# Kernel optimization log

Measured on AMD Instinct MI355X. Metric: run time of the kernel, lower is better.

Reference implementation:

```python
import jax, jax.numpy as jnp
import numpy as np
from jax import lax

K_SQ = 8  # scaling-and-squaring steps (GridExp default)


def lrelu(x):
    return jnp.where(x >= 0, x, 0.2 * x)


def conv(x, w, b, stride=1):
    y = lax.conv_general_dilated(x, w, (stride,) * 3, 'SAME',
                                 dimension_numbers=('NCDHW', 'OIDHW', 'NCDHW'))
    return y + b[None, :, None, None, None]


def convt(x, w, b):
    y = lax.conv_transpose(x, w, (2, 2, 2), 'SAME',
                           dimension_numbers=('NCDHW', 'OIDHW', 'NCDHW'))
    return y + b[None, :, None, None, None]


def identity_grid(shape):
    rng = [jnp.arange(s, dtype=jnp.float32) for s in shape]
    return jnp.stack(jnp.meshgrid(*rng, indexing='ij'), axis=-1)


def pull_one(img, grid, extrapolate):
    # img (C, X, Y, Z); grid (..., 3) in voxel coordinates; trilinear sampling
    X, Y, Z = img.shape[1:]
    g0f = jnp.floor(grid)
    w = grid - g0f
    g0 = g0f.astype(jnp.int32)
    flat = img.reshape(img.shape[0], -1)
    out = jnp.zeros(img.shape[:1] + grid.shape[:-1], img.dtype)
    for dx in (0, 1):
        for dy in (0, 1):
            for dz in (0, 1):
                ix = jnp.clip(g0[..., 0] + dx, 0, X - 1)
                iy = jnp.clip(g0[..., 1] + dy, 0, Y - 1)
                iz = jnp.clip(g0[..., 2] + dz, 0, Z - 1)
                idx = (ix * Y + iy) * Z + iz
                val = jnp.take(flat, idx.reshape(-1), axis=1).reshape(out.shape)
                wgt = ((w[..., 0] if dx else 1 - w[..., 0]) *
                       (w[..., 1] if dy else 1 - w[..., 1]) *
                       (w[..., 2] if dz else 1 - w[..., 2]))
                out = out + wgt[None] * val
    if not extrapolate:  # zero outside the field of view (GridPull extrapolate=False)
        inb = ((grid[..., 0] >= 0) & (grid[..., 0] <= X - 1) &
               (grid[..., 1] >= 0) & (grid[..., 1] <= Y - 1) &
               (grid[..., 2] >= 0) & (grid[..., 2] <= Z - 1))
        out = out * inb[None]
    return out


pull_batch = jax.vmap(pull_one, in_axes=(0, 0, None))


def resize_field(field, out_shape, value_scale):
    # field (B, X, Y, Z, D) channel-last; trilinear resize (align-centers), scale values
    in_shape = field.shape[1:-1]
    coords = identity_grid(out_shape)
    scale = jnp.array([(i - 1) / (o - 1) for i, o in zip(in_shape, out_shape)], jnp.float32)
    coords = coords * scale
    f = jnp.moveaxis(field, -1, 1)
    cb = jnp.broadcast_to(coords, (field.shape[0],) + coords.shape)
    out = pull_batch(f, cb, True)
    return jnp.moveaxis(out, 1, -1) * value_scale


def affine_basis_cso():
    # CSO in 3D: 3 translations + 3 rotations + 1 isotropic zoom -> 7 params
    B = np.zeros((7, 4, 4), np.float32)
    for i in range(3):
        B[i, i, 3] = 1.0
    for k, (i, j) in enumerate([(0, 1), (0, 2), (1, 2)]):
        B[3 + k, i, j] = 1.0
        B[3 + k, j, i] = -1.0
    for i in range(3):
        B[6, i, i] = 1.0
    return jnp.asarray(B)


def forward_core(source, target, cnn_w, cnn_b, enc_w, enc_b, up_w, up_b, dec_w, dec_b, fin_w, fin_b):
    x = jnp.concatenate([source, target], axis=1)  # (B, 2, X, Y, Z)
    # ---- affine head CNN: 4 strided convs + head conv + global reduction -> (B, 7)
    h = x
    for i in range(4):
        h = lrelu(conv(h, cnn_w[i], cnn_b[i], stride=2))
    h = conv(h, cnn_w[4], cnn_b[4])
    aff_prm = h.mean(axis=(2, 3, 4))
    # ---- UNet velocity head -> (B, X, Y, Z, 3)
    skips = [x]
    h = x
    for i in range(4):
        h = lrelu(conv(h, enc_w[i], enc_b[i], stride=2))
        skips.append(h)
    for i in range(4):
        h = lrelu(convt(h, up_w[i], up_b[i]))
        h = jnp.concatenate([h, skips[3 - i]], axis=1)
        h = lrelu(conv(h, dec_w[i], dec_b[i]))
    vel = jnp.moveaxis(conv(h, fin_w, fin_b), 1, -1)
    shape = vel.shape[1:-1]
    small = tuple(s // 2 for s in shape)
    # ---- exp(): downsample velocity (displacement: values scaled by 0.5)
    v_small = resize_field(vel, small, 0.5)
    idg = identity_grid(small)
    d = v_small / (2.0 ** K_SQ)
    for _ in range(K_SQ):  # scaling and squaring: d <- d + d o (id + d)
        d = d + jnp.moveaxis(pull_batch(jnp.moveaxis(d, -1, 1), idg[None] + d, True), 1, -1)
    grid = resize_field(idg[None] + d, shape, 2.0)  # grid: coords scaled by 2
    # ---- affine exponential, re-centered composition
    basis = affine_basis_cso()
    A = jax.vmap(lambda p: jax.scipy.linalg.expm(jnp.einsum('k,kij->ij', p, basis)))(aff_prm)
    shift = jnp.eye(4, dtype=jnp.float32).at[:3, 3].set(-jnp.asarray(shape, jnp.float32) / 2)
    A = jnp.linalg.solve(shift[None], A @ shift[None])  # inv(shift) @ A @ shift
    lin, off = A[:, :3, :3], A[:, :3, 3]
    grid = jnp.einsum('bij,bxyzj->bxyzi', lin, grid) + off[:, None, None, None, :]
    # ---- warp source
    deformed = pull_batch(source, grid, False)
    return deformed, vel, aff_prm


def setup_inputs() -> dict:
    key = jax.random.key(0)
    ks = iter(jax.random.split(key, 48))

    def p(shape):
        return jax.random.normal(next(ks), shape, jnp.float32) * 0.05

    d = {}
    d['source'] = jax.random.normal(next(ks), (1, 1, 96, 96, 96), jnp.float32)
    d['target'] = jax.random.normal(next(ks), (1, 1, 96, 96, 96), jnp.float32)
    for i, (o, c) in enumerate([(16, 2), (32, 16), (32, 32), (32, 32), (7, 32)]):
        d[f'cnn_w{i}'] = p((o, c, 3, 3, 3)); d[f'cnn_b{i}'] = p((o,))
    for i, (o, c) in enumerate([(16, 2), (32, 16), (32, 32), (32, 32)]):
        d[f'enc_w{i}'] = p((o, c, 3, 3, 3)); d[f'enc_b{i}'] = p((o,))
    for i, (o, c) in enumerate([(32, 32), (32, 32), (32, 32), (16, 32)]):
        d[f'up_w{i}'] = p((o, c, 3, 3, 3)); d[f'up_b{i}'] = p((o,))
    for i, (o, c) in enumerate([(32, 64), (32, 64), (32, 48), (16, 18)]):
        d[f'dec_w{i}'] = p((o, c, 3, 3, 3)); d[f'dec_b{i}'] = p((o,))
    d['fin_w'] = p((3, 16, 3, 3, 3)); d['fin_b'] = p((3,))
    return d


def reference(source, target,
              cnn_w0, cnn_b0, cnn_w1, cnn_b1, cnn_w2, cnn_b2, cnn_w3, cnn_b3, cnn_w4, cnn_b4,
              enc_w0, enc_b0, enc_w1, enc_b1, enc_w2, enc_b2, enc_w3, enc_b3,
              up_w0, up_b0, up_w1, up_b1, up_w2, up_b2, up_w3, up_b3,
              dec_w0, dec_b0, dec_w1, dec_b1, dec_w2, dec_b2, dec_w3, dec_b3,
              fin_w, fin_b):
    return forward_core(
        source, target,
        [cnn_w0, cnn_w1, cnn_w2, cnn_w3, cnn_w4], [cnn_b0, cnn_b1, cnn_b2, cnn_b3, cnn_b4],
        [enc_w0, enc_w1, enc_w2, enc_w3], [enc_b0, enc_b1, enc_b2, enc_b3],
        [up_w0, up_w1, up_w2, up_w3], [up_b0, up_b1, up_b2, up_b3],
        [dec_w0, dec_w1, dec_w2, dec_w3], [dec_b0, dec_b1, dec_b2, dec_b3],
        fin_w, fin_b)
```

## Files before the change

### kernel.cpp

```cpp
#include <hip/hip_runtime.h>

#define N96 884736
#define N48 110592
#define N24 13824
#define N12 1728
#define N6  216

typedef __attribute__((ext_vector_type(4))) short short4v;
typedef __attribute__((ext_vector_type(8))) short short8v;
typedef __attribute__((ext_vector_type(4))) float f32x4;

static __device__ __forceinline__ float lrelu_f(float x){ return x >= 0.f ? x : 0.2f*x; }
static __device__ __forceinline__ int clampi(int v,int lo,int hi){ return v<lo?lo:(v>hi?hi:v); }

static __device__ __forceinline__ short f2bf(float x){
    unsigned u = __builtin_bit_cast(unsigned, x);
    unsigned r = (u + 0x7FFFu + ((u >> 16) & 1u)) >> 16;
    return (short)r;
}

template<int OCPB, int S, bool RELU>
static __device__ __forceinline__ void conv_body(
    const float* __restrict__ in1, int C1,
    const float* __restrict__ in2, int C2,
    const float* __restrict__ w, const float* __restrict__ b,
    float* __restrict__ out, int ID, int OD,
    long out_cstride, int out_vmul, int t, int oc0)
{
    int i2 = t % OD; int r = t / OD; int i1 = r % OD; int i0 = r / OD;

    float acc[OCPB];
    #pragma unroll
    for (int j=0; j<OCPB; ++j) acc[j] = b[oc0+j];

    int zz[3], yy[3], xx[3]; bool zv[3], yv[3], xv[3];
    #pragma unroll
    for (int k=0; k<3; ++k){
        int a0 = (S==2) ? (2*i0+k) : (i0+k-1);
        int a1 = (S==2) ? (2*i1+k) : (i1+k-1);
        int a2 = (S==2) ? (2*i2+k) : (i2+k-1);
        zz[k]=a0; zv[k]=(a0>=0)&&(a0<ID);
        yy[k]=a1; yv[k]=(a1>=0)&&(a1<ID);
        xx[k]=a2; xv[k]=(a2>=0)&&(a2<ID);
    }
    const int C = C1 + C2;
    const int ID2 = ID*ID;
    const long ID3 = (long)ID2*ID;

    for (int s=0; s<2; ++s){
        const float* ip = s ? in2 : in1;
        int Cs  = s ? C2 : C1;
        int icb = s ? C1 : 0;
        if (Cs == 0) continue;
        for (int ic=0; ic<Cs; ++ic){
            const float* ipb = ip + (long)ic*ID3;
            float v[27];
            #pragma unroll
            for (int kd=0; kd<3; ++kd)
            #pragma unroll
            for (int kh=0; kh<3; ++kh)
            #pragma unroll
            for (int kw=0; kw<3; ++kw){
                bool ok = zv[kd] && yv[kh] && xv[kw];
                v[kd*9+kh*3+kw] = ok ? ipb[(long)zz[kd]*ID2 + yy[kh]*ID + xx[kw]] : 0.f;
            }
            const float* wbase = w + ((long)oc0*C + (icb+ic))*27;
            #pragma unroll
            for (int j=0; j<OCPB; ++j){
                const float* wo = wbase + (long)j*C*27;
                float sacc = 0.f;
                #pragma unroll
                for (int k=0; k<27; ++k) sacc += wo[k]*v[k];
                acc[j] += sacc;
            }
        }
    }
    #pragma unroll
    for (int j=0; j<OCPB; ++j){
        float o = RELU ? lrelu_f(acc[j]) : acc[j];
        out[(long)(oc0+j)*out_cstride + (long)t*out_vmul] = o;
    }
}

template<int OCPB, int S, bool RELU>
__global__ void conv3d_k(const float* __restrict__ in1, int C1,
                         const float* __restrict__ in2, int C2,
                         const float* __restrict__ w, const float* __restrict__ b,
                         float* __restrict__ out, int ID, int OD,
                         long out_cstride, int out_vmul)
{
    int nvox = OD*OD*OD;
    int t = blockIdx.x*blockDim.x + threadIdx.x;
    if (t >= nvox) return;
    conv_body<OCPB,S,RELU>(in1,C1,in2,C2,w,b,out,ID,OD,out_cstride,out_vmul,t,blockIdx.y*OCPB);
}

template<int OCPB, int S, bool RELU>
__global__ void conv3d_dual_k(const float* __restrict__ in1A, const float* __restrict__ in2A,
                              const float* __restrict__ in1B, const float* __restrict__ in2B,
                              int C1, int C2,
                              const float* __restrict__ wA, const float* __restrict__ bA,
                              const float* __restrict__ wB, const float* __restrict__ bB,
                              float* __restrict__ outA, float* __restrict__ outB,
                              int ID, int OD)
{
    int nvox = OD*OD*OD;
    int t = blockIdx.x*blockDim.x + threadIdx.x;
    if (t >= nvox) return;
    long nv = nvox;
    if (blockIdx.z == 0)
        conv_body<OCPB,S,RELU>(in1A,C1,in2A,C2,wA,bA,outA,ID,OD,nv,1,t,blockIdx.y*OCPB);
    else
        conv_body<OCPB,S,RELU>(in1B,C1,in2B,C2,wB,bB,outB,ID,OD,nv,1,t,blockIdx.y*OCPB);
}

__global__ void e0cl16_k(const float* __restrict__ e0, short* __restrict__ cl){
    int t = blockIdx.x*blockDim.x + threadIdx.x;
    if (t >= N48) return;
    short8v v0, v1;
    #pragma unroll
    for (int c=0;c<8;++c){ v0[c] = f2bf(e0[(long)c*N48 + t]); v1[c] = f2bf(e0[(long)(8+c)*N48 + t]); }
    *(short8v*)(cl + (long)t*16)     = v0;
    *(short8v*)(cl + (long)t*16 + 8) = v1;
}

__global__ __launch_bounds__(256, 2)
void conv_s2mfma_k(const short* __restrict__ cl,
                   const short* __restrict__ pack,
                   const float* __restrict__ b,
                   float* __restrict__ out)
{
    const short8v zero8 = {0,0,0,0,0,0,0,0};
    int lane = threadIdx.x & 63;
    int nb = gridDim.x;
    int bid = blockIdx.x;
    int sb = (bid & 7)*(nb >> 3) + (bid >> 3);
    int wid = sb*4 + (threadIdx.x >> 6);
    int ot = wid & 1;
    int s  = wid >> 1;
    int l15 = lane & 15, g = lane >> 4;
    int vL = s*16 + l15;
    int xL = vL % 24; int rL = vL/24; int yL = rL % 24; int zL = rL/24;
    const bool gok = (g < 2);

    float bias = b[ot*16 + l15];
    f32x4 acc = {bias,bias,bias,bias};

    #pragma unroll
    for (int kz=0; kz<3; ++kz){
        int iz = 2*zL + kz; bool okz = (iz < 48);
        int izc = okz ? iz : 0;
        #pragma unroll
        for (int ky=0; ky<3; ++ky){
            int iy = 2*yL + ky; bool oky = (iy < 48);
            int iyc = oky ? iy : 0;
            #pragma unroll
            for (int kx=0; kx<3; ++kx){
                int ix = 2*xL + kx; bool okx = (ix < 48);
                int ixc = okx ? ix : 0;
                bool ok = okz && oky && okx && gok;
                long base = (((long)izc*48 + iyc)*48 + ixc)*16 + (gok ? 8*g : 0);
                short8v a = *(const short8v*)(cl + base);
                if (!ok) a = zero8;
                int kidx = kz*9 + ky*3 + kx;
                short8v wfr = *(const short8v*)(pack + (((long)ot*27 + kidx)*64 + lane)*8);
                acc = __builtin_amdgcn_mfma_f32_16x16x32_bf16(a, wfr, acc, 0, 0, 0);
            }
        }
    }

    int oc = ot*16 + l15;
    #pragma unroll
    for (int reg=0; reg<4; ++reg){
        int m = 4*g + reg;
        out[(long)oc*N24 + s*16 + m] = lrelu_f(acc[reg]);
    }
}

__global__ void e3cl_k(const float* __restrict__ e3, short* __restrict__ cl){
    int t = blockIdx.x*blockDim.x + threadIdx.x;
    if (t >= N6) return;
    #pragma unroll
    for (int grp=0; grp<4; ++grp){
        short8v v;
        #pragma unroll
        for (int c=0;c<8;++c) v[c] = f2bf(e3[(long)(8*grp+c)*N6 + t]);
        *(short8v*)(cl + (long)t*32 + 8*grp) = v;
    }
}

__global__ void fill_e0_k(const float* __restrict__ e0, short* __restrict__ cl){
    int t = blockIdx.x*blockDim.x + threadIdx.x;
    if (t >= N48) return;
    short8v v0, v1;
    #pragma unroll
    for (int c=0;c<8;++c)  v0[c] = f2bf(e0[(long)c*N48 + t]);
    #pragma unroll
    for (int c=0;c<8;++c)  v1[c] = f2bf(e0[(long)(8+c)*N48 + t]);
    short8v z = {0,0,0,0,0,0,0,0};
    *(short8v*)(cl + (long)t*64 + 32) = v0;
    *(short8v*)(cl + (long)t*64 + 40) = v1;
    *(short8v*)(cl + (long)t*64 + 48) = z;
    *(short8v*)(cl + (long)t*64 + 56) = z;
}

template<int NV>
__global__ void fill_skip32_k(const float* __restrict__ e, short* __restrict__ cl){
    int t = blockIdx.x*blockDim.x + threadIdx.x;
    if (t >= NV) return;
    #pragma unroll
    for (int grp=0; grp<4; ++grp){
        short8v v;
        #pragma unroll
        for (int c=0;c<8;++c) v[c] = f2bf(e[(long)(8*grp+c)*NV + t]);
        *(short8v*)(cl + (long)t*64 + 32 + 8*grp) = v;
    }
}

static __device__ __forceinline__ void pack_std_d(const float* __restrict__ w, short* __restrict__ pack,
                                                  int t, int CREAL, int OCREAL){
    int kidx = t >> 6, lane = t & 63;
    int oc = lane & 15, g = lane >> 4;
    short8v f;
    #pragma unroll
    for (int j=0;j<8;++j){
        int ic = 8*g + j;
        float val = (oc < OCREAL && ic < CREAL) ? w[((long)oc*CREAL + ic)*27 + kidx] : 0.f;
        f[j] = f2bf(val);
    }
    *(short8v*)(pack + (long)t*8) = f;
}
static __device__ __forceinline__ void pack_2x2_d(const float* __restrict__ w, short* __restrict__ pack,
                                                  int t, int C){
    int lane = t & 63;
    int r = t >> 6;
    int kidx = r % 27;
    int kt = (r/27) & 1;
    int ot = r/54;
    int oc = ot*16 + (lane & 15), g = lane >> 4;
    short8v f;
    #pragma unroll
    for (int j=0;j<8;++j){
        int ic = kt*32 + 8*g + j;
        float val = (ic < C) ? w[((long)oc*C + ic)*27 + kidx] : 0.f;
        f[j] = f2bf(val);
    }
    *(short8v*)(pack + (long)t*8) = f;
}
static __device__ __forceinline__ void pack_up_d(const float* __restrict__ w, short* __restrict__ pack, int t){
    int lane = t & 63;
    int r = t >> 6;
    int kidx = r % 27;
    int ot = r/27;
    int oc = ot*16 + (lane & 15), g = lane >> 4;
    short8v f;
    #pragma unroll
    for (int j=0;j<8;++j){
        int ic = 8*g + j;
        f[j] = f2bf(w[((long)oc*32 + ic)*27 + kidx]);
    }
    *(short8v*)(pack + (long)t*8) = f;
}
static __device__ __forceinline__ void pack_s2_d(const float* __restrict__ w, short* __restrict__ pack, int t){
    int lane = t & 63;
    int r = t >> 6;
    int kidx = r % 27;
    int ot = r/27;
    int oc = ot*16 + (lane & 15), g = lane >> 4;
    short8v f;
    #pragma unroll
    for (int j=0;j<8;++j){
        int ic = 8*g + j;
        float val = (ic < 16) ? w[((long)oc*16 + ic)*27 + kidx] : 0.f;
        f[j] = f2bf(val);
    }
    *(short8v*)(pack + (long)t*8) = f;
}

__global__ void pack_all_k(const float* __restrict__ dw3, const float* __restrict__ fw,
                           const float* __restrict__ uw3,
                           const float* __restrict__ dw2, const float* __restrict__ dw1,
                           const float* __restrict__ dw0,
                           const float* __restrict__ uw2, const float* __restrict__ uw1,
                           const float* __restrict__ uw0,
                           const float* __restrict__ ew1,
                           short* __restrict__ PK3, short* __restrict__ PKF, short* __restrict__ PKU,
                           short* __restrict__ PK2, short* __restrict__ PK1, short* __restrict__ PK0,
                           short* __restrict__ PKU2, short* __restrict__ PKU1, short* __restrict__ PKU0,
                           short* __restrict__ PKE1)
{
    int t = blockIdx.x*blockDim.x + threadIdx.x;
    const int S1 = 27*64;
    const int S4 = 4*27*64;
    const int S2 = 2*27*64;
    if (t < S1){ pack_std_d(dw3, PK3, t, 18, 16); return; } t -= S1;
    if (t < S1){ pack_std_d(fw,  PKF, t, 16,  3); return; } t -= S1;
    if (t < S1){ pack_std_d(uw3, PKU, t, 32, 16); return; } t -= S1;
    if (t < S4){ pack_2x2_d(dw2, PK2, t, 48); return; } t -= S4;
    if (t < S4){ pack_2x2_d(dw1, PK1, t, 64); return; } t -= S4;
    if (t < S4){ pack_2x2_d(dw0, PK0, t, 64); return; } t -= S4;
    if (t < S2){ pack_up_d(uw2, PKU2, t); return; } t -= S2;
    if (t < S2){ pack_up_d(uw1, PKU1, t); return; } t -= S2;
    if (t < S2){ pack_up_d(uw0, PKU0, t); return; } t -= S2;
    if (t < S2){ pack_s2_d(ew1, PKE1, t); return; }
}

template<int CSTR, int OCREAL, bool RELU, int OMODE>
__global__ __launch_bounds__(256, 4)
void conv_mfma2_k(const short* __restrict__ cl,
                  const short* __restrict__ pack,
                  const float* __restrict__ b,
                  void* __restrict__ outp)
{
    const int D2 = 96*96;
    const short8v zero8 = {0,0,0,0,0,0,0,0};
    __shared__ short lwfr[27*64*8];
    for (int idx = threadIdx.x; idx < 27*64; idx += 256)
        *(short8v*)(lwfr + (long)idx*8) = *(const short8v*)(pack + (long)idx*8);
    __syncthreads();

    int lane = threadIdx.x & 63;
    int nb = gridDim.x;
    int bid = blockIdx.x;
    int sb = (bid & 7)*(nb >> 3) + (bid >> 3);
    int wid = sb*4 + (threadIdx.x >> 6);
    int l15 = lane & 15, g = lane >> 4;
    int xh = wid & 1;
    int rem = wid >> 1;
    int y = rem % 96;
    int z = (rem / 96)*2;
    int x0b = xh*48;
    const bool gok = (8*g < CSTR);
    const int go = gok ? 8*g : 0;

    float bias = (l15 < OCREAL) ? b[l15] : 0.f;
    f32x4 acc[2][3];
    #pragma unroll
    for (int o=0;o<2;++o)
    #pragma unroll
    for (int i=0;i<3;++i) acc[o][i] = (f32x4){bias,bias,bias,bias};

    #pragma unroll
    for (int dzr=-1; dzr<=2; ++dzr){
        int zz = z + dzr;
        bool okz = (zz>=0) && (zz<96);
        int zc = okz ? zz : z;
        #pragma unroll
        for (int dy=-1; dy<=1; ++dy){
            int yy = y+dy;
            bool okrow = okz && (yy>=0) && (yy<96);
            int yc = (yy>=0 && yy<96) ? yy : y;
            long rowb = (long)zc*D2 + (long)yc*96;
            #pragma unroll
            for (int dx=-1; dx<=1; ++dx){
                short8v a[3];
                #pragma unroll
                for (int i=0;i<3;++i){
                    int x = x0b + 16*i + l15 + dx;
                    bool okx = (x>=0) && (x<96);
                    int xc = okx ? x : (x0b + 16*i + l15);
                    a[i] = *(const short8v*)(cl + (rowb + xc)*CSTR + go);
                    bool oka = okrow && okx && gok;
                    if (!oka) a[i] = zero8;
                }
                if (dzr >= -1 && dzr <= 1){
                    int kidx = (dzr+1)*9 + (dy+1)*3 + (dx+1);
                    short8v wfr = *(const short8v*)(lwfr + ((long)kidx*64 + lane)*8);
                    #pragma unroll
                    for (int i=0;i<3;++i)
                        acc[0][i] = __builtin_amdgcn_mfma_f32_16x16x32_bf16(a[i], wfr, acc[0][i], 0, 0, 0);
                }
                if (dzr >= 0 && dzr <= 2){
                    int kidx = (dzr)*9 + (dy+1)*3 + (dx+1);
                    short8v wfr = *(const short8v*)(lwfr + ((long)kidx*64 + lane)*8);
                    #pragma unroll
                    for (int i=0;i<3;++i)
                        acc[1][i] = __builtin_amdgcn_mfma_f32_16x16x32_bf16(a[i], wfr, acc[1][i], 0, 0, 0);
                }
            }
        }
    }

    #pragma unroll
    for (int o=0;o<2;++o){
        long vrow = (long)(z+o)*D2 + (long)y*96 + x0b;
        if (OMODE == 0){
            short* op = (short*)outp;
            #pragma unroll
            for (int i=0;i<3;++i)
            #pragma unroll
            for (int reg=0; reg<4; ++reg){
                int mr = 4*g + reg;
                float v = RELU ? lrelu_f(acc[o][i][reg]) : acc[o][i][reg];
                op[(vrow + 16*i + mr)*16 + l15] = f2bf(v);
            }
        } else {
            float* op = (float*)outp;
            if (l15 < 3){
                #pragma unroll
                for (int i=0;i<3;++i)
                #pragma unroll
                for (int reg=0; reg<4; ++reg){
                    int mr = 4*g + reg;
                    op[(vrow + 16*i + mr)*3 + l15] = acc[o][i][reg];
                }
            }
        }
    }
}

__global__ __launch_bounds__(256, 2)
void conv_mfma48_k(const short* __restrict__ cl,
                   const short* __restrict__ pack,
                   const float* __restrict__ b,
                   short* __restrict__ out)
{
    const int D2 = 48*48;
    const short8v zero8 = {0,0,0,0,0,0,0,0};
    int lane = threadIdx.x & 63;
    int nb = gridDim.x;
    int bid = blockIdx.x;
    int sb = (bid & 7)*(nb >> 3) + (bid >> 3);
    int wid = sb*4 + (threadIdx.x >> 6);
    int l15 = lane & 15, g = lane >> 4;
    int y = wid % 48, z = wid / 48;

    float bias0 = b[l15];
    float bias1 = b[16 + l15];
    f32x4 acc[2][3];
    #pragma unroll
    for (int i=0;i<3;++i){ acc[0][i] = (f32x4){bias0,bias0,bias0,bias0};
                           acc[1][i] = (f32x4){bias1,bias1,bias1,bias1}; }

    #pragma unroll
    for (int dz=-1; dz<=1; ++dz){
        int zz = z+dz;
        bool okz = (zz>=0) && (zz<48);
        int zc = okz ? zz : z;
        #pragma unroll
        for (int dy=-1; dy<=1; ++dy){
            int yy = y+dy;
            bool okzy = okz && (yy>=0) && (yy<48);
            int yc = (yy>=0 && yy<48) ? yy : y;
            long rowb = (long)zc*D2 + (long)yc*48;
            #pragma unroll
            for (int dx=-1; dx<=1; ++dx){
                int kidx = (dz+1)*9 + (dy+1)*3 + (dx+1);
                #pragma unroll
                for (int kt=0; kt<2; ++kt){
                    short8v a[3];
                    #pragma unroll
                    for (int i=0;i<3;++i){
                        int x = 16*i + l15 + dx;
                        bool okx = (x>=0) && (x<48);
                        int xc = okx ? x : (16*i + l15);
                        a[i] = *(const short8v*)(cl + ((rowb + xc)*64 + kt*32 + 8*g));
                        if (!okx) a[i] = zero8;
                    }
                    #pragma unroll
                    for (int ot=0; ot<2; ++ot){
                        short8v wfr = *(const short8v*)(pack + (((long)(ot*2+kt)*27 + kidx)*64 + lane)*8);
                        if (!okzy) wfr = zero8;
                        #pragma unroll
                        for (int i=0;i<3;++i)
                            acc[ot][i] = __builtin_amdgcn_mfma_f32_16x16x32_bf16(a[i], wfr, acc[ot][i], 0, 0, 0);
                    }
                }
            }
        }
    }

    long vrow = (long)z*D2 + (long)y*48;
    #pragma unroll
    for (int ot=0; ot<2; ++ot)
    #pragma unroll
    for (int i=0;i<3;++i)
    #pragma unroll
    for (int reg=0; reg<4; ++reg){
        int mr = 4*g + reg;
        out[(vrow + 16*i + mr)*32 + ot*16 + l15] = f2bf(lrelu_f(acc[ot][i][reg]));
    }
}

template<int D>
__global__ __launch_bounds__(256, 2)
void conv_mfmaD_k(const short* __restrict__ cl,
                  const short* __restrict__ pack,
                  const float* __restrict__ b,
                  short* __restrict__ out)
{
    const short8v zero8 = {0,0,0,0,0,0,0,0};
    int lane = threadIdx.x & 63;
    int nb = gridDim.x;
    int bid = blockIdx.x;
    int sb = ((nb & 7) == 0) ? ((bid & 7)*(nb >> 3) + (bid >> 3)) : bid;
    int wid = sb*4 + (threadIdx.x >> 6);
    int ot = wid & 1;
    int s  = wid >> 1;
    int l15 = lane & 15, g = lane >> 4;
    int vL = s*16 + l15;
    int xL = vL % D; int rL = vL/D; int yL = rL % D; int zL = rL/D;

    float bias = b[ot*16 + l15];
    f32x4 acc = {bias,bias,bias,bias};

    #pragma unroll
    for (int dz=-1; dz<=1; ++dz){
        int iz = zL+dz; bool okz = (iz>=0)&&(iz<D); int izc = okz?iz:zL;
        #pragma unroll
        for (int dy=-1; dy<=1; ++dy){
            int iy = yL+dy; bool oky = (iy>=0)&&(iy<D); int iyc = oky?iy:yL;
            #pragma unroll
            for (int dx=-1; dx<=1; ++dx){
                int ix = xL+dx; bool okx = (ix>=0)&&(ix<D); int ixc = okx?ix:xL;
                bool ok = okz && oky && okx;
                long base = (((long)izc*D + iyc)*D + ixc)*64;
                int kidx = (dz+1)*9 + (dy+1)*3 + (dx+1);
                #pragma unroll
                for (int kt=0; kt<2; ++kt){
                    short8v wfr = *(const short8v*)(pack + (((long)(ot*2+kt)*27 + kidx)*64 + lane)*8);
                    short8v a = *(const short8v*)(cl + base + kt*32 + 8*g);
                    if (!ok) a = zero8;
                    acc = __builtin_amdgcn_mfma_f32_16x16x32_bf16(a, wfr, acc, 0, 0, 0);
                }
            }
        }
    }

    #pragma unroll
    for (int reg=0; reg<4; ++reg){
        int m = 4*g + reg;
        out[(long)(s*16 + m)*32 + ot*16 + l15] = f2bf(lrelu_f(acc[reg]));
    }
}

template<int IDI, int NST>
__global__ __launch_bounds__(256, 2)
void convt_mfmaup_k(const short* __restrict__ cl,
                    const short* __restrict__ pack,
                    const float* __restrict__ b,
                    short* __restrict__ o)
{
    const int D2i = IDI*IDI;
    const int OD = 2*IDI;
    const long D2o = (long)OD*OD;
    int lane = threadIdx.x & 63;
    int nb = gridDim.x;
    int bid = blockIdx.x;
    int sb = ((nb & 7) == 0) ? ((bid & 7)*(nb >> 3) + (bid >> 3)) : bid;
    int wid = sb*4 + (threadIdx.x >> 6);
    int px = wid & 1;
    int row = wid >> 1;
    int y = row % OD, z = row / OD;
    int l15 = lane & 15, g = lane >> 4;
    int pz = z & 1, py = y & 1, hz = z >> 1, hy = y >> 1;

    float bias0 = b[l15], bias1 = b[16 + l15];
    f32x4 acc[2][NST];
    #pragma unroll
    for (int i=0;i<NST;++i){ acc[0][i] = (f32x4){bias0,bias0,bias0,bias0};
                             acc[1][i] = (f32x4){bias1,bias1,bias1,bias1}; }

    int k0s[2], izs[2], nz=0;
    if (pz){ k0s[0]=1; izs[0]=hz; nz=1; }
    else { if (hz>=1){ k0s[nz]=0; izs[nz]=hz-1; ++nz; } k0s[nz]=2; izs[nz]=hz; ++nz; }
    int k1s[2], iys[2], ny=0;
    if (py){ k1s[0]=1; iys[0]=hy; ny=1; }
    else { if (hy>=1){ k1s[ny]=0; iys[ny]=hy-1; ++ny; } k1s[ny]=2; iys[ny]=hy; ++ny; }

    for (int a=0;a<nz;++a)
    for (int c=0;c<ny;++c){
        long rowb = (long)izs[a]*D2i + (long)iys[c]*IDI;
        int kbase = k0s[a]*9 + k1s[c]*3;
        int nqx = px?1:2;
        for (int qx=0; qx<nqx; ++qx){
            int k2 = px ? 1 : 2*qx;
            int xoff = px ? 0 : (qx-1);
            short8v av[NST];
            #pragma unroll
            for (int i=0;i<NST;++i){
                int ix = 16*i + l15 + xoff;
                av[i] = (short8v){0,0,0,0,0,0,0,0};
                if (ix >= 0 && ix < IDI) av[i] = *(const short8v*)(cl + ((rowb + ix)*32 + 8*g));
            }
            #pragma unroll
            for (int ot=0; ot<2; ++ot){
                short8v wfr = *(const short8v*)(pack + (((long)ot*27 + kbase + k2)*64 + lane)*8);
                #pragma unroll
                for (int i=0;i<NST;++i)
                    acc[ot][i] = __builtin_amdgcn_mfma_f32_16x16x32_bf16(av[i], wfr, acc[ot][i], 0, 0, 0);
            }
        }
    }

    #pragma unroll
    for (int ot=0; ot<2; ++ot)
    #pragma unroll
    for (int i=0;i<NST;++i)
    #pragma unroll
    for (int reg=0; reg<4; ++reg){
        int m = 16*i + 4*g + reg;
        if (m < IDI){
            long vox = (long)z*D2o + (long)y*OD + (2*m + px);
            o[vox*64 + ot*16 + l15] = f2bf(lrelu_f(acc[ot][i][reg]));
        }
    }
}

__global__ __launch_bounds__(256, 2)
void convt_mfma96_k(const short* __restrict__ cl,
                    const short* __restrict__ pack,
                    const float* __restrict__ b,
                    const float* __restrict__ src,
                    const float* __restrict__ tgt,
                    short* __restrict__ o)
{
    const int D2i = 48*48;
    const long D2o = 96*96;
    int lane = threadIdx.x & 63;
    int nb = gridDim.x;
    int bid = blockIdx.x;
    int sb = (bid & 7)*(nb >> 3) + (bid >> 3);
    int wid = sb*4 + (threadIdx.x >> 6);
    int px = wid & 1;
    int row = wid >> 1;
    int y = row % 96, z = row / 96;
    int l15 = lane & 15, g = lane >> 4;
    int pz = z & 1, py = y & 1, hz = z >> 1, hy = y >> 1;

    float bias = b[l15];
    f32x4 acc[3];
    #pragma unroll
    for (int i=0;i<3;++i) acc[i] = (f32x4){bias,bias,bias,bias};

    int k0s[2], izs[2], nz=0;
    if (pz){ k0s[0]=1; izs[0]=hz; nz=1; }
    else { if (hz>=1){ k0s[nz]=0; izs[nz]=hz-1; ++nz; } k0s[nz]=2; izs[nz]=hz; ++nz; }
    int k1s[2], iys[2], ny=0;
    if (py){ k1s[0]=1; iys[0]=hy; ny=1; }
    else { if (hy>=1){ k1s[ny]=0; iys[ny]=hy-1; ++ny; } k1s[ny]=2; iys[ny]=hy; ++ny; }

    for (int a=0;a<nz;++a)
    for (int c=0;c<ny;++c){
        long rowb = (long)izs[a]*D2i + (long)iys[c]*48;
        int kbase = k0s[a]*9 + k1s[c]*3;
        int nqx = px?1:2;
        for (int qx=0; qx<nqx; ++qx){
            int k2 = px ? 1 : 2*qx;
            int xoff = px ? 0 : (qx-1);
            short8v wfr = *(const short8v*)(pack + ((long)(kbase+k2)*64 + lane)*8);
            #pragma unroll
            for (int i=0;i<3;++i){
                int ix = 16*i + l15 + xoff;
                short8v av = {0,0,0,0,0,0,0,0};
                if (ix >= 0) av = *(const short8v*)(cl + ((rowb + ix)*32 + 8*g));
                acc[i] = __builtin_amdgcn_mfma_f32_16x16x32_bf16(av, wfr, acc[i], 0, 0, 0);
            }
        }
    }

    #pragma unroll
    for (int i=0;i<3;++i)
    #pragma unroll
    for (int reg=0; reg<4; ++reg){
        int m = 16*i + 4*g + reg;
        long vox = (long)z*D2o + (long)y*96 + (2*m + px);
        o[vox*24 + l15] = f2bf(lrelu_f(acc[i][reg]));
        if (l15 == 0)      o[vox*24 + 16] = f2bf(src[vox]);
        else if (l15 == 1) o[vox*24 + 17] = f2bf(tgt[vox]);
        else if (l15 < 8)  o[vox*24 + 16 + l15] = 0;
    }
}

static __device__ void mat4mul(const double* A, const double* B, double* C){
    for (int i=0;i<4;++i) for (int j=0;j<4;++j){
        double s=0; for (int k=0;k<4;++k) s += A[i*4+k]*B[k*4+j];
        C[i*4+j]=s;
    }
}

__global__ void affine_k(const float* __restrict__ c4, float* __restrict__ aff_out, float* __restrict__ mats){
    __shared__ float p[7];
    int t = threadIdx.x;
    if (t < 7){
        float s = 0.f;
        for (int i=0;i<N6;++i) s += c4[t*N6 + i];
        p[t] = s / (float)N6;
        aff_out[t] = p[t];
    }
    __syncthreads();
    if (t == 0){
        double M[16];
        for (int i=0;i<16;++i) M[i]=0.0;
        M[0*4+3]=p[0]; M[1*4+3]=p[1]; M[2*4+3]=p[2];
        M[0*4+1]= p[3]; M[1*4+0]=-p[3];
        M[0*4+2]= p[4]; M[2*4+0]=-p[4];
        M[1*4+2]= p[5]; M[2*4+1]=-p[5];
        M[0*4+0]+=p[6]; M[1*4+1]+=p[6]; M[2*4+2]+=p[6];
        double nrm=0.0;
        for (int i=0;i<4;++i){
            double s=0; for (int j=0;j<4;++j) s += fabs(M[i*4+j]);
            if (s>nrm) nrm=s;
        }
        int jj=0;
        while (nrm > 0.25 && jj < 40){ nrm *= 0.5; ++jj; }
        double sc = 1.0; for (int q=0;q<jj;++q) sc *= 0.5;
        double Ms[16]; for (int i=0;i<16;++i) Ms[i]=M[i]*sc;
        double E[16], T[16], Tn[16];
        for (int i=0;i<16;++i){ E[i] = (i%5==0)?1.0:0.0; T[i]=E[i]; }
        for (int k=1;k<=18;++k){
            mat4mul(T, Ms, Tn);
            double inv = 1.0/(double)k;
            for (int i=0;i<16;++i){ T[i]=Tn[i]*inv; E[i]+=T[i]; }
        }
        for (int q=0;q<jj;++q){ mat4mul(E,E,Tn); for (int i=0;i<16;++i) E[i]=Tn[i]; }
        const double tsh = -48.0;
        for (int i=0;i<3;++i){
            for (int j=0;j<3;++j) mats[i*3+j] = (float)E[i*4+j];
            double rs = (E[i*4+0] - (i==0?1.0:0.0))
                      + (E[i*4+1] - (i==1?1.0:0.0))
                      + (E[i*4+2] - (i==2?1.0:0.0));
            mats[9+i] = (float)(E[i*4+3] + rs*tsh);
        }
    }
}

static __device__ __forceinline__ void trilerp3(const float* __restrict__ f, int D,
                                                float c0, float c1, float c2, float out3[3]){
    float f0=floorf(c0), f1=floorf(c1), f2=floorf(c2);
    float w0=c0-f0, w1=c1-f1, w2=c2-f2;
    int a0=(int)f0, a1=(int)f1, a2=(int)f2;
    int i0s[2]={clampi(a0,0,D-1), clampi(a0+1,0,D-1)};
    int i1s[2]={clampi(a1,0,D-1), clampi(a1+1,0,D-1)};
    int i2s[2]={clampi(a2,0,D-1), clampi(a2+1,0,D-1)};
    float w0s[2]={1.f-w0,w0}, w1s[2]={1.f-w1,w1}, w2s[2]={1.f-w2,w2};
    out3[0]=out3[1]=out3[2]=0.f;
    #pragma unroll
    for (int dx=0;dx<2;++dx)
    #pragma unroll
    for (int dy=0;dy<2;++dy)
    #pragma unroll
    for (int dz=0;dz<2;++dz){
        float wg = w0s[dx]*w1s[dy]*w2s[dz];
        const float* pp = f + ((i0s[dx]*D + i1s[dy])*D + i2s[dz])*3;
        out3[0]+=wg*pp[0]; out3[1]+=wg*pp[1]; out3[2]+=wg*pp[2];
    }
}

static __device__ __forceinline__ float trilerp1(const float* __restrict__ f, int D,
                                                 float c0, float c1, float c2){
    float f0=floorf(c0), f1=floorf(c1), f2=floorf(c2);
    float w0=c0-f0, w1=c1-f1, w2=c2-f2;
    int a0=(int)f0, a1=(int)f1, a2=(int)f2;
    int i0s[2]={clampi(a0,0,D-1), clampi(a0+1,0,D-1)};
    int i1s[2]={clampi(a1,0,D-1), clampi(a1+1,0,D-1)};
    int i2s[2]={clampi(a2,0,D-1), clampi(a2+1,0,D-1)};
    float w0s[2]={1.f-w0,w0}, w1s[2]={1.f-w1,w1}, w2s[2]={1.f-w2,w2};
    float s=0.f;
    #pragma unroll
    for (int dx=0;dx<2;++dx)
    #pragma unroll
    for (int dy=0;dy<2;++dy)
    #pragma unroll
    for (int dz=0;dz<2;++dz){
        float wg = w0s[dx]*w1s[dy]*w2s[dz];
        s += wg * f[(i0s[dx]*D + i1s[dy])*D + i2s[dz]];
    }
    return s;
}

__global__ void resize_small_k(const float* __restrict__ vel, float* __restrict__ dA){
    int t = blockIdx.x*blockDim.x + threadIdx.x;
    if (t >= N48) return;
    int i2 = t % 48; int r = t / 48; int i1 = r % 48; int i0 = r / 48;
    const float s = 95.f/47.f;
    float o[3];
    trilerp3(vel, 96, i0*s, i1*s, i2*s, o);
    const float k = 0.5f/256.f;
    dA[t*3+0]=o[0]*k; dA[t*3+1]=o[1]*k; dA[t*3+2]=o[2]*k;
}

__global__ void sq_k(const float* __restrict__ din, float* __restrict__ dout){
    int t = blockIdx.x*blockDim.x + threadIdx.x;
    if (t >= N48) return;
    int i2 = t % 48; int r = t / 48; int i1 = r % 48; int i0 = r / 48;
    float d0=din[t*3+0], d1=din[t*3+1], d2=din[t*3+2];
    float s[3];
    trilerp3(din, 48, (float)i0+d0, (float)i1+d1, (float)i2+d2, s);
    dout[t*3+0]=d0+s[0]; dout[t*3+1]=d1+s[1]; dout[t*3+2]=d2+s[2];
}

__global__ void grid_pull_k(const float* __restrict__ dfin, const float* __restrict__ src,
                            const float* __restrict__ mats, float* __restrict__ out){
    int t = blockIdx.x*blockDim.x + threadIdx.x;
    if (t >= N96) return;
    int i2 = t % 96; int r = t / 96; int i1 = r % 96; int i0 = r / 96;
    const float sc = 47.f/95.f;
    float c0=i0*sc, c1=i1*sc, c2=i2*sc;
    float s[3];
    trilerp3(dfin, 48, c0, c1, c2, s);
    float g0 = 2.f*(c0+s[0]), g1 = 2.f*(c1+s[1]), g2 = 2.f*(c2+s[2]);
    float L00=mats[0],L01=mats[1],L02=mats[2],L10=mats[3],L11=mats[4],L12=mats[5],
          L20=mats[6],L21=mats[7],L22=mats[8],o0=mats[9],o1=mats[10],o2=mats[11];
    float gg0 = L00*g0 + L01*g1 + L02*g2 + o0;
    float gg1 = L10*g0 + L11*g1 + L12*g2 + o1;
    float gg2 = L20*g0 + L21*g1 + L22*g2 + o2;
    bool inb = (gg0>=0.f)&&(gg0<=95.f)&&(gg1>=0.f)&&(gg1<=95.f)&&(gg2>=0.f)&&(gg2<=95.f);
    float val = trilerp1(src, 96, gg0, gg1, gg2);
    out[t] = inb ? val : 0.f;
}

extern "C" void kernel_launch(void* const* d_in, const int* in_sizes, int n_in,
                              void* d_out, int out_size, void* d_ws, size_t ws_size,
                              hipStream_t stream) {
    const float* src = (const float*)d_in[0];
    const float* tgt = (const float*)d_in[1];
    const float *cw[5], *cb[5], *ew[4], *eb[4], *uw[4], *ub[4], *dw[4], *db[4];
    for (int i=0;i<5;++i){ cw[i]=(const float*)d_in[2+2*i]; cb[i]=(const float*)d_in[3+2*i]; }
    for (int i=0;i<4;++i){ ew[i]=(const float*)d_in[12+2*i]; eb[i]=(const float*)d_in[13+2*i]; }
    for (int i=0;i<4;++i){ uw[i]=(const float*)d_in[20+2*i]; ub[i]=(const float*)d_in[21+2*i]; }
    for (int i=0;i<4;++i){ dw[i]=(const float*)d_in[28+2*i]; db[i]=(const float*)d_in[29+2*i]; }
    const float* fw = (const float*)d_in[36];
    const float* fb = (const float*)d_in[37];

    float* ws = (float*)d_ws;
    const long OFF_E0 = 0;
    const long OFF_CLE0 = OFF_E0 + 16L*N48;
    const long OFF_E1 = OFF_CLE0 + 8L*N48;
    const long OFF_E2 = OFF_E1 + 32L*N24;
    const long OFF_E3 = OFF_E2 + 32L*N12;
    const long OFF_B1 = OFF_E3 + 32L*N6;
    const long OFF_B2 = OFF_B1 + 32L*N48;
    const long OFF_CL24 = OFF_B2 + 32L*N48;
    const long OFF_CL16 = OFF_CL24 + 12L*N96;
    const long OFF_DA = OFF_CL16 + 8L*N96;
    const long OFF_DB = OFF_DA + 3L*N48;
    const long OFF_MT = OFF_DB + 3L*N48;
    const long OFF_PK3 = OFF_MT + 16;
    const long OFF_PKF = OFF_PK3 + 6912;
    const long OFF_PK2 = OFF_PKF + 6912;
    const long OFF_PKU = OFF_PK2 + 27648;
    const long OFF_PK1 = OFF_PKU + 6912;
    const long OFF_PK0 = OFF_PK1 + 27648;
    const long OFF_PKU2 = OFF_PK0 + 27648;
    const long OFF_PKU1 = OFF_PKU2 + 13824;
    const long OFF_PKU0 = OFF_PKU1 + 13824;
    const long OFF_PKE1 = OFF_PKU0 + 13824;
    const long OFF_CLD2 = OFF_PKE1 + 13824;
    const long OFF_CL64B = OFF_CLD2 + 16L*N48;
    const long OFF_CLD1 = OFF_CL64B + 32L*N24;
    const long OFF_CL64C = OFF_CLD1 + 16L*N24;
    const long OFF_CLD0 = OFF_CL64C + 32L*N12;
    const long OFF_CLE3 = OFF_CLD0 + 16L*N12;
    const long WS_TOT = OFF_CLE3 + 16L*N6;
    if (ws_size < (size_t)WS_TOT*4) return;

    float* E0 = ws + OFF_E0;
    short* CLE0 = (short*)(ws + OFF_CLE0);
    float* E1 = ws + OFF_E1;
    float* E2 = ws + OFF_E2;
    float* E3 = ws + OFF_E3;
    float* B1 = ws + OFF_B1;
    float* B2 = ws + OFF_B2;
    short* CL24 = (short*)(ws + OFF_CL24);
    short* CL16 = (short*)(ws + OFF_CL16);
    short* CL64 = (short*)(ws + OFF_CL16);
    float* DA = ws + OFF_DA;
    float* DB = ws + OFF_DB;
    float* MT = ws + OFF_MT;
    short* PK3 = (short*)(ws + OFF_PK3);
    short* PKF = (short*)(ws + OFF_PKF);
    short* PK2 = (short*)(ws + OFF_PK2);
    short* PKU = (short*)(ws + OFF_PKU);
    short* PK1 = (short*)(ws + OFF_PK1);
    short* PK0 = (short*)(ws + OFF_PK0);
    short* PKU2 = (short*)(ws + OFF_PKU2);
    short* PKU1 = (short*)(ws + OFF_PKU1);
    short* PKU0 = (short*)(ws + OFF_PKU0);
    short* PKE1 = (short*)(ws + OFF_PKE1);
    short* CLD2 = (short*)(ws + OFF_CLD2);
    short* CL64B = (short*)(ws + OFF_CL64B);
    short* CLD1 = (short*)(ws + OFF_CLD1);
    short* CL64C = (short*)(ws + OFF_CL64C);
    short* CLD0 = (short*)(ws + OFF_CLD0);
    short* CLE3 = (short*)(ws + OFF_CLE3);

    float* out_def = (float*)d_out;
    float* out_vel = out_def + N96;
    float* out_aff = out_vel + 3L*N96;

    auto gsz = [](int n, int b){ return (n + b - 1)/b; };

    pack_all_k<<<gsz(39744,256), 256, 0, stream>>>(dw[3], fw, uw[3], dw[2], dw[1], dw[0],
                                                   uw[2], uw[1], uw[0], ew[1],
                                                   PK3, PKF, PKU, PK2, PK1, PK0,
                                                   PKU2, PKU1, PKU0, PKE1);

    conv3d_dual_k< 8,2,true><<<dim3(gsz(N48,256), 2,2), 256, 0, stream>>>(src,tgt, src,tgt, 1,1, cw[0],cb[0], ew[0],eb[0], B1,E0, 96,48);

    e0cl16_k<<<gsz(N48,256), 256, 0, stream>>>(E0, CLE0);

    conv3d_k< 4,2,true><<<dim3(gsz(N24,256), 8), 256, 0, stream>>>(B1,16, nullptr,0, cw[1],cb[1], B2, 48,24, N24, 1);
    conv_s2mfma_k<<<432, 256, 0, stream>>>(CLE0, PKE1, eb[1], E1);

    conv3d_dual_k< 2,2,true><<<dim3(gsz(N12, 64),16,2),  64, 0, stream>>>(B2,nullptr, E1,nullptr, 32,0, cw[2],cb[2], ew[2],eb[2], B1,E2, 24,12);
    conv3d_dual_k< 1,2,true><<<dim3(gsz(N6 , 64),32,2),  64, 0, stream>>>(B1,nullptr, E2,nullptr, 32,0, cw[3],cb[3], ew[3],eb[3], B2,E3, 12, 6);
    conv3d_k< 1,1,false><<<dim3(gsz(N6 , 64), 7), 64, 0, stream>>>(B2,32, nullptr, 0, cw[4], cb[4], B1, 6, 6, N6, 1);
    affine_k<<<1, 64, 0, stream>>>(B1, out_aff, MT);

    e3cl_k<<<1, 256, 0, stream>>>(E3, CLE3);

    convt_mfmaup_k<6,1><<<72, 256, 0, stream>>>(CLE3, PKU0, ub[0], CL64C);
    fill_skip32_k<N12><<<gsz(N12,256), 256, 0, stream>>>(E2, CL64C);

    conv_mfmaD_k<12><<<54, 256, 0, stream>>>(CL64C, PK0, db[0], CLD0);

    convt_mfmaup_k<12,1><<<288, 256, 0, stream>>>(CLD0, PKU1, ub[1], CL64B);
    fill_skip32_k<N24><<<gsz(N24,256), 256, 0, stream>>>(E1, CL64B);

    conv_mfmaD_k<24><<<432, 256, 0, stream>>>(CL64B, PK1, db[1], CLD1);

    convt_mfmaup_k<24,2><<<1152, 256, 0, stream>>>(CLD1, PKU2, ub[2], CL64);
    fill_e0_k<<<gsz(N48,256), 256, 0, stream>>>(E0, CL64);

    conv_mfma48_k<<<576, 256, 0, stream>>>(CL64, PK2, db[2], CLD2);

    convt_mfma96_k<<<4608, 256, 0, stream>>>(CLD2, PKU, ub[3], src, tgt, CL24);

    conv_mfma2_k<24,16,true ,0><<<2304, 256, 0, stream>>>(CL24, PK3, db[3], (void*)CL16);
    conv_mfma2_k<16, 3,false,1><<<2304, 256, 0, stream>>>(CL16, PKF, fb, (void*)out_vel);

    resize_small_k<<<gsz(N48,256), 256, 0, stream>>>(out_vel, DA);
    float* da = DA; float* dbuf = DB;
    for (int it=0; it<8; ++it){
        sq_k<<<gsz(N48,256), 256, 0, stream>>>(da, dbuf);
        float* tmp = da; da = dbuf; dbuf = tmp;
    }

    grid_pull_k<<<gsz(N96,256), 256, 0, stream>>>(da, src, MT, out_def);
}
```

Before: 498.3 us.

## Split 48^3 decoder conv so each wave computes one 16-voxel x-segment

The 48^3 decoder convolution now assigns one 16-voxel segment of a row to each wave instead of a whole 48-voxel row. This triples the grid to 1728 blocks and raises the launch-bounds occupancy hint from 2 to 4. Accumulator and register pressure drop, which is meant to allow more resident waves and better latency hiding. In exchange, each weight fragment is reloaded three times as often because it is no longer reused across three M-tiles, and out-of-bounds handling now zeroes the activations rather than the weights.

```diff
diff --git a/kernel.cpp b/kernel.cpp
--- a/kernel.cpp
+++ b/kernel.cpp
@@ -409,7 +409,7 @@
     }
 }
 
-__global__ __launch_bounds__(256, 2)
+__global__ __launch_bounds__(256, 4)
 void conv_mfma48_k(const short* __restrict__ cl,
                    const short* __restrict__ pack,
                    const float* __restrict__ b,
@@ -423,14 +423,15 @@
     int sb = (bid & 7)*(nb >> 3) + (bid >> 3);
     int wid = sb*4 + (threadIdx.x >> 6);
     int l15 = lane & 15, g = lane >> 4;
-    int y = wid % 48, z = wid / 48;
+    int s3 = wid % 3;
+    int row = wid / 3;
+    int y = row % 48, z = row / 48;
+    int x0 = s3*16 + l15;
 
     float bias0 = b[l15];
     float bias1 = b[16 + l15];
-    f32x4 acc[2][3];
-    #pragma unroll
-    for (int i=0;i<3;++i){ acc[0][i] = (f32x4){bias0,bias0,bias0,bias0};
-                           acc[1][i] = (f32x4){bias1,bias1,bias1,bias1}; }
+    f32x4 acc0 = {bias0,bias0,bias0,bias0};
+    f32x4 acc1 = {bias1,bias1,bias1,bias1};
 
     #pragma unroll
     for (int dz=-1; dz<=1; ++dz){
@@ -445,40 +446,33 @@
             long rowb = (long)zc*D2 + (long)yc*48;
             #pragma unroll
             for (int dx=-1; dx<=1; ++dx){
+                int x = x0 + dx;
+                bool okx = (x>=0) && (x<48);
+                int xc = okx ? x : x0;
+                bool ok = okzy && okx;
+                long base = (rowb + xc)*64 + 8*g;
+                short8v a0 = *(const short8v*)(cl + base);
+                short8v a1 = *(const short8v*)(cl + base + 32);
+                if (!ok){ a0 = zero8; a1 = zero8; }
                 int kidx = (dz+1)*9 + (dy+1)*3 + (dx+1);
-                #pragma unroll
-                for (int kt=0; kt<2; ++kt){
-                    short8v a[3];
-                    #pragma unroll
-                    for (int i=0;i<3;++i){
-                        int x = 16*i + l15 + dx;
-                        bool okx = (x>=0) && (x<48);
-                        int xc = okx ? x : (16*i + l15);
-                        a[i] = *(const short8v*)(cl + ((rowb + xc)*64 + kt*32 + 8*g));
-                        if (!okx) a[i] = zero8;
-                    }
-                    #pragma unroll
-                    for (int ot=0; ot<2; ++ot){
-                        short8v wfr = *(const short8v*)(pack + (((long)(ot*2+kt)*27 + kidx)*64 + lane)*8);
-                        if (!okzy) wfr = zero8;
-                        #pragma unroll
-                        for (int i=0;i<3;++i)
-                            acc[ot][i] = __builtin_amdgcn_mfma_f32_16x16x32_bf16(a[i], wfr, acc[ot][i], 0, 0, 0);
-                    }
-                }
-            }
-        }
-    }
-
-    long vrow = (long)z*D2 + (long)y*48;
-    #pragma unroll
-    for (int ot=0; ot<2; ++ot)
-    #pragma unroll
-    for (int i=0;i<3;++i)
+                short8v w00 = *(const short8v*)(pack + (((long)(0*2+0)*27 + kidx)*64 + lane)*8);
+                short8v w01 = *(const short8v*)(pack + (((long)(0*2+1)*27 + kidx)*64 + lane)*8);
+                short8v w10 = *(const short8v*)(pack + (((long)(1*2+0)*27 + kidx)*64 + lane)*8);
+                short8v w11 = *(const short8v*)(pack + (((long)(1*2+1)*27 + kidx)*64 + lane)*8);
+                acc0 = __builtin_amdgcn_mfma_f32_16x16x32_bf16(a0, w00, acc0, 0, 0, 0);
+                acc0 = __builtin_amdgcn_mfma_f32_16x16x32_bf16(a1, w01, acc0, 0, 0, 0);
+                acc1 = __builtin_amdgcn_mfma_f32_16x16x32_bf16(a0, w10, acc1, 0, 0, 0);
+                acc1 = __builtin_amdgcn_mfma_f32_16x16x32_bf16(a1, w11, acc1, 0, 0, 0);
+            }
+        }
+    }
+
+    long vrow = (long)z*D2 + (long)y*48 + s3*16;
     #pragma unroll
     for (int reg=0; reg<4; ++reg){
         int mr = 4*g + reg;
-        out[(vrow + 16*i + mr)*32 + ot*16 + l15] = f2bf(lrelu_f(acc[ot][i][reg]));
+        out[(vrow + mr)*32 + l15]      = f2bf(lrelu_f(acc0[reg]));
+        out[(vrow + mr)*32 + 16 + l15] = f2bf(lrelu_f(acc1[reg]));
     }
 }
 
@@ -923,7 +917,7 @@
     convt_mfmaup_k<24,2><<<1152, 256, 0, stream>>>(CLD1, PKU2, ub[2], CL64);
     fill_e0_k<<<gsz(N48,256), 256, 0, stream>>>(E0, CL64);
 
-    conv_mfma48_k<<<576, 256, 0, stream>>>(CL64, PK2, db[2], CLD2);
+    conv_mfma48_k<<<1728, 256, 0, stream>>>(CL64, PK2, db[2], CLD2);
 
     convt_mfma96_k<<<4608, 256, 0, stream>>>(CLD2, PKU, ub[3], src, tgt, CL24);
 
```

After: 499.0 us. No clear change (+0.1%).

## Split 48^3 conv output channels across grid.y and stage weights in LDS

Applied to the files above, without the earlier changes.

The 48^3 decoder conv now launches twice as many blocks, each handling one 16-channel output tile selected by blockIdx.y. Each block copies its slice of packed weights into shared memory and reads weight fragments from LDS instead of global memory. Per-wave accumulator count halves, which should ease register pressure and raise parallelism. In exchange, activation loads are duplicated across the two channel halves and each block pays an upfront weight copy plus a barrier. The zero-padding mask is now applied to activations rather than weights.

```diff
diff --git a/kernel.cpp b/kernel.cpp
--- a/kernel.cpp
+++ b/kernel.cpp
@@ -417,6 +417,12 @@
 {
     const int D2 = 48*48;
     const short8v zero8 = {0,0,0,0,0,0,0,0};
+    __shared__ short lwfr[2*27*64*8];
+    int ot = blockIdx.y;
+    for (int idx = threadIdx.x; idx < 2*27*64; idx += 256)
+        *(short8v*)(lwfr + (long)idx*8) = *(const short8v*)(pack + ((long)ot*2*27*64 + idx)*8);
+    __syncthreads();
+
     int lane = threadIdx.x & 63;
     int nb = gridDim.x;
     int bid = blockIdx.x;
@@ -425,12 +431,10 @@
     int l15 = lane & 15, g = lane >> 4;
     int y = wid % 48, z = wid / 48;
 
-    float bias0 = b[l15];
-    float bias1 = b[16 + l15];
-    f32x4 acc[2][3];
-    #pragma unroll
-    for (int i=0;i<3;++i){ acc[0][i] = (f32x4){bias0,bias0,bias0,bias0};
-                           acc[1][i] = (f32x4){bias1,bias1,bias1,bias1}; }
+    float bias = b[ot*16 + l15];
+    f32x4 acc[3];
+    #pragma unroll
+    for (int i=0;i<3;++i) acc[i] = (f32x4){bias,bias,bias,bias};
 
     #pragma unroll
     for (int dz=-1; dz<=1; ++dz){
@@ -446,39 +450,32 @@
             #pragma unroll
             for (int dx=-1; dx<=1; ++dx){
                 int kidx = (dz+1)*9 + (dy+1)*3 + (dx+1);
+                short8v wfr0 = *(const short8v*)(lwfr + (((long)0*27 + kidx)*64 + lane)*8);
+                short8v wfr1 = *(const short8v*)(lwfr + (((long)1*27 + kidx)*64 + lane)*8);
                 #pragma unroll
-                for (int kt=0; kt<2; ++kt){
-                    short8v a[3];
-                    #pragma unroll
-                    for (int i=0;i<3;++i){
-                        int x = 16*i + l15 + dx;
-                        bool okx = (x>=0) && (x<48);
-                        int xc = okx ? x : (16*i + l15);
-                        a[i] = *(const short8v*)(cl + ((rowb + xc)*64 + kt*32 + 8*g));
-                        if (!okx) a[i] = zero8;
-                    }
-                    #pragma unroll
-                    for (int ot=0; ot<2; ++ot){
-                        short8v wfr = *(const short8v*)(pack + (((long)(ot*2+kt)*27 + kidx)*64 + lane)*8);
-                        if (!okzy) wfr = zero8;
-                        #pragma unroll
-                        for (int i=0;i<3;++i)
-                            acc[ot][i] = __builtin_amdgcn_mfma_f32_16x16x32_bf16(a[i], wfr, acc[ot][i], 0, 0, 0);
-                    }
+                for (int i=0;i<3;++i){
+                    int x = 16*i + l15 + dx;
+                    bool okx = (x>=0) && (x<48);
+                    int xc = okx ? x : (16*i + l15);
+                    bool ok = okzy && okx;
+                    long base = (rowb + xc)*64 + 8*g;
+                    short8v a0 = *(const short8v*)(cl + base);
+                    short8v a1 = *(const short8v*)(cl + base + 32);
+                    if (!ok){ a0 = zero8; a1 = zero8; }
+                    acc[i] = __builtin_amdgcn_mfma_f32_16x16x32_bf16(a0, wfr0, acc[i], 0, 0, 0);
+                    acc[i] = __builtin_amdgcn_mfma_f32_16x16x32_bf16(a1, wfr1, acc[i], 0, 0, 0);
                 }
             }
         }
     }
 
     long vrow = (long)z*D2 + (long)y*48;
-    #pragma unroll
-    for (int ot=0; ot<2; ++ot)
     #pragma unroll
     for (int i=0;i<3;++i)
     #pragma unroll
     for (int reg=0; reg<4; ++reg){
         int mr = 4*g + reg;
-        out[(vrow + 16*i + mr)*32 + ot*16 + l15] = f2bf(lrelu_f(acc[ot][i][reg]));
+        out[(vrow + 16*i + mr)*32 + ot*16 + l15] = f2bf(lrelu_f(acc[i][reg]));
     }
 }
 
@@ -923,7 +920,7 @@
     convt_mfmaup_k<24,2><<<1152, 256, 0, stream>>>(CLD1, PKU2, ub[2], CL64);
     fill_e0_k<<<gsz(N48,256), 256, 0, stream>>>(E0, CL64);
 
-    conv_mfma48_k<<<576, 256, 0, stream>>>(CL64, PK2, db[2], CLD2);
+    conv_mfma48_k<<<dim3(576,2), 256, 0, stream>>>(CL64, PK2, db[2], CLD2);
 
     convt_mfma96_k<<<4608, 256, 0, stream>>>(CLD2, PKU, ub[3], src, tgt, CL24);
 
```

Result: slower. 530.2 us (+6.4%).

## Shrink 48^3 decoder channel-last buffer stride from 64 to 48 channels

Applied to the files above, without the earlier changes.

The concatenated 48-channel activation at 48^3 was stored padded to 64 channels with explicit zero fill. It now uses a 48-channel stride: the upsampling conv writes with stride 48, fill_e0 no longer writes the zero padding, and conv_mfma48 loads the second K half only for lane groups 0-1 and zeroes the rest. This cuts memory footprint and traffic for that buffer, at the cost of less aligned row strides and some masked lane loads.

```diff
diff --git a/kernel.cpp b/kernel.cpp
--- a/kernel.cpp
+++ b/kernel.cpp
@@ -197,11 +197,8 @@
     for (int c=0;c<8;++c)  v0[c] = f2bf(e0[(long)c*N48 + t]);
     #pragma unroll
     for (int c=0;c<8;++c)  v1[c] = f2bf(e0[(long)(8+c)*N48 + t]);
-    short8v z = {0,0,0,0,0,0,0,0};
-    *(short8v*)(cl + (long)t*64 + 32) = v0;
-    *(short8v*)(cl + (long)t*64 + 40) = v1;
-    *(short8v*)(cl + (long)t*64 + 48) = z;
-    *(short8v*)(cl + (long)t*64 + 56) = z;
+    *(short8v*)(cl + (long)t*48 + 32) = v0;
+    *(short8v*)(cl + (long)t*48 + 40) = v1;
 }
 
 template<int NV>
@@ -424,6 +421,8 @@
     int wid = sb*4 + (threadIdx.x >> 6);
     int l15 = lane & 15, g = lane >> 4;
     int y = wid % 48, z = wid / 48;
+    const bool g1ok = (g < 2);
+    const int go1 = g1ok ? (32 + 8*g) : 0;
 
     float bias0 = b[l15];
     float bias1 = b[16 + l15];
@@ -446,24 +445,27 @@
             #pragma unroll
             for (int dx=-1; dx<=1; ++dx){
                 int kidx = (dz+1)*9 + (dy+1)*3 + (dx+1);
+                short8v a0[3], a1[3];
                 #pragma unroll
-                for (int kt=0; kt<2; ++kt){
-                    short8v a[3];
+                for (int i=0;i<3;++i){
+                    int x = 16*i + l15 + dx;
+                    bool okx = (x>=0) && (x<48);
+                    int xc = okx ? x : (16*i + l15);
+                    bool ok = okzy && okx;
+                    long base = (rowb + xc)*48;
+                    a0[i] = *(const short8v*)(cl + base + 8*g);
+                    a1[i] = *(const short8v*)(cl + base + go1);
+                    if (!ok) a0[i] = zero8;
+                    if (!(ok && g1ok)) a1[i] = zero8;
+                }
+                #pragma unroll
+                for (int ot=0; ot<2; ++ot){
+                    short8v wfr0 = *(const short8v*)(pack + (((long)(ot*2+0)*27 + kidx)*64 + lane)*8);
+                    short8v wfr1 = *(const short8v*)(pack + (((long)(ot*2+1)*27 + kidx)*64 + lane)*8);
                     #pragma unroll
                     for (int i=0;i<3;++i){
-                        int x = 16*i + l15 + dx;
-                        bool okx = (x>=0) && (x<48);
-                        int xc = okx ? x : (16*i + l15);
-                        a[i] = *(const short8v*)(cl + ((rowb + xc)*64 + kt*32 + 8*g));
-                        if (!okx) a[i] = zero8;
-                    }
-                    #pragma unroll
-                    for (int ot=0; ot<2; ++ot){
-                        short8v wfr = *(const short8v*)(pack + (((long)(ot*2+kt)*27 + kidx)*64 + lane)*8);
-                        if (!okzy) wfr = zero8;
-                        #pragma unroll
-                        for (int i=0;i<3;++i)
-                            acc[ot][i] = __builtin_amdgcn_mfma_f32_16x16x32_bf16(a[i], wfr, acc[ot][i], 0, 0, 0);
+                        acc[ot][i] = __builtin_amdgcn_mfma_f32_16x16x32_bf16(a0[i], wfr0, acc[ot][i], 0, 0, 0);
+                        acc[ot][i] = __builtin_amdgcn_mfma_f32_16x16x32_bf16(a1[i], wfr1, acc[ot][i], 0, 0, 0);
                     }
                 }
             }
@@ -534,7 +536,7 @@
     }
 }
 
-template<int IDI, int NST>
+template<int IDI, int NST, int OSTR>
 __global__ __launch_bounds__(256, 2)
 void convt_mfmaup_k(const short* __restrict__ cl,
                     const short* __restrict__ pack,
@@ -602,7 +604,7 @@
         int m = 16*i + 4*g + reg;
         if (m < IDI){
             long vox = (long)z*D2o + (long)y*OD + (2*m + px);
-            o[vox*64 + ot*16 + l15] = f2bf(lrelu_f(acc[ot][i][reg]));
+            o[vox*OSTR + ot*16 + l15] = f2bf(lrelu_f(acc[ot][i][reg]));
         }
     }
 }
@@ -864,7 +866,7 @@
     float* B2 = ws + OFF_B2;
     short* CL24 = (short*)(ws + OFF_CL24);
     short* CL16 = (short*)(ws + OFF_CL16);
-    short* CL64 = (short*)(ws + OFF_CL16);
+    short* CL48 = (short*)(ws + OFF_CL16);
     float* DA = ws + OFF_DA;
     float* DB = ws + OFF_DB;
     float* MT = ws + OFF_MT;
@@ -910,20 +912,20 @@
 
     e3cl_k<<<1, 256, 0, stream>>>(E3, CLE3);
 
-    convt_mfmaup_k<6,1><<<72, 256, 0, stream>>>(CLE3, PKU0, ub[0], CL64C);
+    convt_mfmaup_k<6,1,64><<<72, 256, 0, stream>>>(CLE3, PKU0, ub[0], CL64C);
     fill_skip32_k<N12><<<gsz(N12,256), 256, 0, stream>>>(E2, CL64C);
 
     conv_mfmaD_k<12><<<54, 256, 0, stream>>>(CL64C, PK0, db[0], CLD0);
 
-    convt_mfmaup_k<12,1><<<288, 256, 0, stream>>>(CLD0, PKU1, ub[1], CL64B);
+    convt_mfmaup_k<12,1,64><<<288, 256, 0, stream>>>(CLD0, PKU1, ub[1], CL64B);
     fill_skip32_k<N24><<<gsz(N24,256), 256, 0, stream>>>(E1, CL64B);
 
     conv_mfmaD_k<24><<<432, 256, 0, stream>>>(CL64B, PK1, db[1], CLD1);
 
-    convt_mfmaup_k<24,2><<<1152, 256, 0, stream>>>(CLD1, PKU2, ub[2], CL64);
-    fill_e0_k<<<gsz(N48,256), 256, 0, stream>>>(E0, CL64);
-
-    conv_mfma48_k<<<576, 256, 0, stream>>>(CL64, PK2, db[2], CLD2);
+    convt_mfmaup_k<24,2,48><<<1152, 256, 0, stream>>>(CLD1, PKU2, ub[2], CL48);
+    fill_e0_k<<<gsz(N48,256), 256, 0, stream>>>(E0, CL48);
+
+    conv_mfma48_k<<<576, 256, 0, stream>>>(CL48, PK2, db[2], CLD2);
 
     convt_mfma96_k<<<4608, 256, 0, stream>>>(CLD2, PKU, ub[3], src, tgt, CL24);
 
```

Measured after the change: 465.8 us, median of 2. 6.5% less time.
